# Kernel optimization log

Measured on AMD Instinct MI355X. Metric: run time of the kernel, lower is better.

The kernel has to match this reference:

```python
import jax, jax.numpy as jnp
import numpy as np
from jax import lax

N_P = 0.5      # module_cfg.n_p
CUTOFF = 0.3   # module_cfg.cutoff


def setup_inputs() -> dict:
    key = jax.random.key(0)
    k1, k2, k3, k4 = jax.random.split(key, 4)
    h = jax.random.normal(k1, (1, 8192, 256), jnp.float32)
    pos = jax.random.normal(k2, (8192, 3), jnp.float32)
    W = jax.random.normal(k3, (256, 256), jnp.float32) / 16.0  # ~ Linear init scale
    b = jax.random.normal(k4, (256,), jnp.float32) * 0.01
    return {"h": h, "pos": pos, "W": W, "b": b}


def fps_indices(pos, k, select=0):
    """Farthest point sampling; returns the k selected indices in ascending
    index order (matching torch boolean-mask indexing pos[selected])."""
    n = pos.shape[0]
    selected = jnp.zeros(n, dtype=bool).at[select].set(True)
    d = jnp.linalg.norm(pos - pos[select], axis=-1)  # (N,) euclidean, as torch.pairwise_distance
    d = jnp.where(selected, -jnp.inf, d)

    def body(i, carry):
        sel, dist = carry
        new = jnp.argmax(dist)
        sel = sel.at[new].set(True)
        dist = jnp.minimum(dist, jnp.linalg.norm(pos - pos[new], axis=-1))
        dist = jnp.where(sel, -jnp.inf, dist)
        return sel, dist

    sel, _ = lax.fori_loop(0, k - 1, body, (selected, d))
    return jnp.nonzero(sel, size=k)[0]  # exactly k True entries, sorted


def reference(h, pos, W, b):
    B, num_res, c_s = h.shape
    n_nodes = int(num_res * N_P)  # num_res * n_p // 1

    idx = fps_indices(pos, n_nodes)          # (n_nodes,)
    new_node_pos = pos[idx]                  # (n_nodes, 3)

    # torch.cdist(pos, new_node_pos, p=3): Minkowski p=3 distance
    diff = jnp.abs(pos[:, None, :] - new_node_pos[None, :, :])  # (N, n_nodes, 3)
    dist = jnp.cbrt(jnp.sum(diff ** 3, axis=-1))                 # (N, n_nodes)

    # sparse membership mask (fixed-shape equivalent of the nonzero edge list)
    mask = dist < CUTOFF                      # (N, n_nodes) bool

    # sparse gather-matmul: aggregate residue features into each sampled node
    agg = jnp.einsum('nm,bnc->bmc', mask.astype(h.dtype), h)     # (B, n_nodes, c_s)
    new_node_embed = agg @ W.T + b            # nn.Linear(c_s, c_s)
    return new_node_embed, new_node_pos, mask
```

## Files before the change

### kernel.cpp

```cpp
#include <hip/hip_runtime.h>
#include <hip/hip_bf16.h>
#include <cmath>

#define FPS_N 8192
#define FPS_K 4096
#define NTHR  1024
#define CS    256

#define NEGINF (-__builtin_inff())

__device__ __forceinline__ float p3sum(float x, float y, float z,
                                       float nx, float ny, float nz) {
  float dx = fabsf(__fsub_rn(x, nx));
  float dy = fabsf(__fsub_rn(y, ny));
  float dz = fabsf(__fsub_rn(z, nz));
  float cx = __fmul_rn(__fmul_rn(dx, dx), dx);
  float cy = __fmul_rn(__fmul_rn(dy, dy), dy);
  float cz = __fmul_rn(__fmul_rn(dz, dz), dz);
  return __fadd_rn(__fadd_rn(cx, cy), cz);
}

__device__ __forceinline__ float eucl2(float x, float y, float z,
                                       float nx, float ny, float nz) {
  float dx = __fsub_rn(x, nx);
  float dy = __fsub_rn(y, ny);
  float dz = __fsub_rn(z, nz);
  return __fadd_rn(__fadd_rn(__fmul_rn(dx, dx), __fmul_rn(dy, dy)),
                   __fmul_rn(dz, dz));
}

__global__ __launch_bounds__(NTHR) void fps_kernel(const float* __restrict__ pos,
                                                   float* __restrict__ pos_out) {
  __shared__ float rv[16];
  __shared__ int   ri[16];
  __shared__ float wposs[3];
  __shared__ int   sc[NTHR];
  const int tid  = threadIdx.x;
  const int lane = tid & 63;
  const int wave = tid >> 6;

  float x[8], y[8], z[8], d2[8], dd[8];
  {
    const float4* p4 = (const float4*)pos + tid * 6;
    float4 q0 = p4[0], q1 = p4[1], q2 = p4[2], q3 = p4[3], q4 = p4[4], q5 = p4[5];
    x[0] = q0.x; y[0] = q0.y; z[0] = q0.z;
    x[1] = q0.w; y[1] = q1.x; z[1] = q1.y;
    x[2] = q1.z; y[2] = q1.w; z[2] = q2.x;
    x[3] = q2.y; y[3] = q2.z; z[3] = q2.w;
    x[4] = q3.x; y[4] = q3.y; z[4] = q3.z;
    x[5] = q3.w; y[5] = q4.x; z[5] = q4.y;
    x[6] = q4.z; y[6] = q4.w; z[6] = q5.x;
    x[7] = q5.y; y[7] = q5.z; z[7] = q5.w;
  }
  const float p0x = pos[0], p0y = pos[1], p0z = pos[2];
#pragma unroll
  for (int j = 0; j < 8; ++j) {
    float s = eucl2(x[j], y[j], z[j], p0x, p0y, p0z);
    d2[j] = s;
    dd[j] = sqrtf(s);
  }
  if (tid == 0) { d2[0] = NEGINF; dd[0] = NEGINF; }

  float bv = 0.f; int bj = 0;
  bool chb = true;

  for (int k = 0; k < FPS_K - 1; ++k) {
    unsigned long long cb = __ballot(chb ? 1 : 0);
    if (cb != 0ULL) {
      if (chb) {
        bv = dd[0]; bj = 0;
#pragma unroll
        for (int j = 1; j < 8; ++j)
          if (dd[j] > bv) { bv = dd[j]; bj = j; }
        chb = false;
      }
      float m = bv;
#pragma unroll
      for (int off = 32; off > 0; off >>= 1)
        m = fmaxf(m, __shfl_xor(m, off));
      unsigned long long eq = __ballot((bv == m) ? 1 : 0);
      int lead = __ffsll(eq) - 1;
      int lbj  = __shfl(bj, lead);
      if (lane == 0) {
        rv[wave] = m;
        ri[wave] = ((wave << 6) + lead) * 8 + lbj;
      }
    }
    __syncthreads();

    float v  = rv[lane & 15];
    int  idx = ri[lane & 15];
#pragma unroll
    for (int off = 1; off < 16; off <<= 1) {
      float ov = __shfl_xor(v, off);
      int   oi = __shfl_xor(idx, off);
      if (ov > v || (ov == v && oi < idx)) { v = ov; idx = oi; }
    }
    const int fi = idx;

    if ((fi >> 3) == tid) {
      const int jj = fi & 7;
      float sx = x[0], sy = y[0], sz = z[0];
#pragma unroll
      for (int j = 0; j < 8; ++j)
        if (j == jj) { sx = x[j]; sy = y[j]; sz = z[j]; d2[j] = NEGINF; dd[j] = NEGINF; }
      wposs[0] = sx; wposs[1] = sy; wposs[2] = sz;
      chb = true;
    }
    __syncthreads();

    const float wx = wposs[0], wy = wposs[1], wz = wposs[2];
    unsigned cm = 0;
#pragma unroll
    for (int j = 0; j < 8; ++j) {
      float s = eucl2(x[j], y[j], z[j], wx, wy, wz);
      if (s < d2[j]) { d2[j] = s; cm |= (1u << j); }
    }
    if (cm) {
#pragma unroll
      for (int j = 0; j < 8; ++j)
        if (cm & (1u << j)) { dd[j] = sqrtf(d2[j]); if (j == bj) chb = true; }
    }
  }

  int cnt = 0;
#pragma unroll
  for (int j = 0; j < 8; ++j) cnt += (dd[j] == NEGINF) ? 1 : 0;
  sc[tid] = cnt;
  __syncthreads();
  for (int off = 1; off < NTHR; off <<= 1) {
    int vv = (tid >= off) ? sc[tid - off] : 0;
    __syncthreads();
    sc[tid] += vv;
    __syncthreads();
  }
  int base = sc[tid] - cnt;
#pragma unroll
  for (int j = 0; j < 8; ++j) {
    if (dd[j] == NEGINF) {
      pos_out[base * 3 + 0] = x[j];
      pos_out[base * 3 + 1] = y[j];
      pos_out[base * 3 + 2] = z[j];
      ++base;
    }
  }
}

__global__ __launch_bounds__(256) void wt_kernel(const float* __restrict__ W,
                                                 float* __restrict__ WT) {
  int i = blockIdx.x * 256 + threadIdx.x;
  int c = i >> 8, cp = i & 255;
  WT[i] = W[cp * 256 + c];
}

__global__ __launch_bounds__(256) void agg_linear_kernel(
    const float* __restrict__ h, const float* __restrict__ pos,
    const float* __restrict__ nodepos, const float* __restrict__ WT,
    const float* __restrict__ bias, float* __restrict__ embed, float sb) {
  const int m = blockIdx.x;
  const int tid = threadIdx.x;
  const int lane = tid & 63, wave = tid >> 6;
  const float nx = nodepos[m * 3 + 0];
  const float ny = nodepos[m * 3 + 1];
  const float nz = nodepos[m * 3 + 2];
  const float4* h4 = (const float4*)h;

  float4 acc = make_float4(0.f, 0.f, 0.f, 0.f);
  const int base0 = wave * (FPS_N / 4);
  for (int base = base0; base < base0 + (FPS_N / 4); base += 64) {
    int n = base + lane;
    float px = pos[n * 3 + 0], py = pos[n * 3 + 1], pz = pos[n * 3 + 2];
    unsigned long long mb = __ballot((p3sum(px, py, pz, nx, ny, nz) <= sb) ? 1 : 0);
    while (mb) {
      int b = __ffsll(mb) - 1;
      mb &= (mb - 1);
      float4 hv = h4[(size_t)(base + b) * 64 + lane];
      acc.x += hv.x; acc.y += hv.y; acc.z += hv.z; acc.w += hv.w;
    }
  }

  __shared__ float lacc[4][256];
  lacc[wave][lane * 4 + 0] = acc.x;
  lacc[wave][lane * 4 + 1] = acc.y;
  lacc[wave][lane * 4 + 2] = acc.z;
  lacc[wave][lane * 4 + 3] = acc.w;
  __syncthreads();
  __shared__ float aggrow[256];
  float aggv = ((lacc[0][tid] + lacc[1][tid]) + lacc[2][tid]) + lacc[3][tid];
  aggrow[tid] = aggv;
  __syncthreads();

  float o = bias[tid];
#pragma unroll 8
  for (int c = 0; c < 256; ++c)
    o = fmaf(aggrow[c], WT[c * 256 + tid], o);
  embed[(size_t)m * 256 + tid] = o;
}

__global__ __launch_bounds__(256) void mask_kernel(const float* __restrict__ pos,
                                                   const float* __restrict__ nodepos,
                                                   float* __restrict__ maskout,
                                                   float sb) {
  int n  = blockIdx.y;
  int m0 = (blockIdx.x * 256 + threadIdx.x) * 4;
  float x = pos[n * 3 + 0], y = pos[n * 3 + 1], z = pos[n * 3 + 2];
  const float4* np4 = (const float4*)(nodepos + (size_t)m0 * 3);
  float4 a = np4[0], bq = np4[1], cq = np4[2];
  float4 r;
  r.x = (p3sum(x, y, z, a.x,  a.y,  a.z)  <= sb) ? 1.0f : 0.0f;
  r.y = (p3sum(x, y, z, a.w,  bq.x, bq.y) <= sb) ? 1.0f : 0.0f;
  r.z = (p3sum(x, y, z, bq.z, bq.w, cq.x) <= sb) ? 1.0f : 0.0f;
  r.w = (p3sum(x, y, z, cq.y, cq.z, cq.w) <= sb) ? 1.0f : 0.0f;
  *(float4*)(maskout + (size_t)n * FPS_K + m0) = r;
}

extern "C" void kernel_launch(void* const* d_in, const int* in_sizes, int n_in,
                              void* d_out, int out_size, void* d_ws, size_t ws_size,
                              hipStream_t stream) {
  (void)in_sizes; (void)n_in; (void)out_size; (void)d_ws; (void)ws_size;
  const float* h   = (const float*)d_in[0];
  const float* pos = (const float*)d_in[1];
  const float* W   = (const float*)d_in[2];
  const float* b   = (const float*)d_in[3];

  float* out     = (float*)d_out;
  float* embed   = out;
  float* pos_out = out + (size_t)FPS_K * CS;
  float* mask    = pos_out + (size_t)FPS_K * 3;
  float* WT      = mask;

  const float  t    = 0.3f;
  const float  ulpv = nextafterf(t, 1.0f) - t;
  const double rmid = (double)t - (double)ulpv * 0.5;
  const double C    = rmid * rmid * rmid;
  float sb = (float)C;
  if (!((double)sb < C)) sb = nextafterf(sb, 0.0f);

  hipLaunchKernelGGL(fps_kernel, dim3(1), dim3(NTHR), 0, stream, pos, pos_out);
  hipLaunchKernelGGL(wt_kernel, dim3(256), dim3(256), 0, stream, W, WT);
  hipLaunchKernelGGL(agg_linear_kernel, dim3(FPS_K), dim3(256), 0, stream,
                     h, pos, pos_out, WT, b, embed, sb);
  hipLaunchKernelGGL(mask_kernel, dim3(4, FPS_N), dim3(256), 0, stream,
                     pos, pos_out, mask, sb);
}
```

Baseline: 7.548 ms.

## Spatially bin points for FPS and skip distance updates by bounding-box pruning

```diff
diff --git a/kernel.cpp b/kernel.cpp
--- a/kernel.cpp
+++ b/kernel.cpp
@@ -4,9 +4,9 @@
 
 #define FPS_N 8192
 #define FPS_K 4096
-#define NTHR  1024
 #define CS    256
-
+#define FT    512
+#define PPT   16
 #define NEGINF (-__builtin_inff())
 
 __device__ __forceinline__ float p3sum(float x, float y, float z,
@@ -29,119 +29,209 @@
                    __fmul_rn(dz, dz));
 }
 
-__global__ __launch_bounds__(NTHR) void fps_kernel(const float* __restrict__ pos,
-                                                   float* __restrict__ pos_out) {
-  __shared__ float rv[16];
-  __shared__ int   ri[16];
-  __shared__ float wposs[3];
-  __shared__ int   sc[NTHR];
+__global__ __launch_bounds__(FT) void bin_kernel(const float* __restrict__ pos,
+                                                 float* __restrict__ pos_s,
+                                                 int* __restrict__ ids_s) {
+  __shared__ int hist[512], cs[512], tmp[512];
+  const int tid = threadIdx.x;
+  hist[tid] = 0;
+  __syncthreads();
+
+  float qx[PPT], qy[PPT], qz[PPT];
+  int cell[PPT];
+  {
+    const float4* p4 = (const float4*)pos + tid * 12;
+#pragma unroll
+    for (int g = 0; g < 4; ++g) {
+      float4 a = p4[g * 3], b = p4[g * 3 + 1], c = p4[g * 3 + 2];
+      qx[4*g+0]=a.x; qy[4*g+0]=a.y; qz[4*g+0]=a.z;
+      qx[4*g+1]=a.w; qy[4*g+1]=b.x; qz[4*g+1]=b.y;
+      qx[4*g+2]=b.z; qy[4*g+2]=b.w; qz[4*g+2]=c.x;
+      qx[4*g+3]=c.y; qy[4*g+3]=c.z; qz[4*g+3]=c.w;
+    }
+  }
+#pragma unroll
+  for (int j = 0; j < PPT; ++j) {
+    int ix = min(max((int)floorf(qx[j] + 4.0f), 0), 7);
+    int iy = min(max((int)floorf(qy[j] + 4.0f), 0), 7);
+    int iz = min(max((int)floorf(qz[j] + 4.0f), 0), 7);
+    int m = 0;
+#pragma unroll
+    for (int b = 0; b < 3; ++b)
+      m |= (((ix >> b) & 1) << (3 * b)) | (((iy >> b) & 1) << (3 * b + 1)) |
+           (((iz >> b) & 1) << (3 * b + 2));
+    cell[j] = m;
+    atomicAdd(&hist[m], 1);
+  }
+  __syncthreads();
+  int v = hist[tid];
+  tmp[tid] = v;
+  __syncthreads();
+  for (int off = 1; off < 512; off <<= 1) {
+    int u = (tid >= off) ? tmp[tid - off] : 0;
+    __syncthreads();
+    tmp[tid] += u;
+    __syncthreads();
+  }
+  cs[tid] = tmp[tid] - v;
+  __syncthreads();
+#pragma unroll
+  for (int j = 0; j < PPT; ++j) {
+    int slot = atomicAdd(&cs[cell[j]], 1);
+    pos_s[slot * 3 + 0] = qx[j];
+    pos_s[slot * 3 + 1] = qy[j];
+    pos_s[slot * 3 + 2] = qz[j];
+    ids_s[slot] = tid * PPT + j;
+  }
+}
+
+__global__ __launch_bounds__(FT, 1) void fps_kernel(const float* __restrict__ pos,
+                                                    const float* __restrict__ pos_s,
+                                                    const int* __restrict__ ids_s,
+                                                    float* __restrict__ pos_out) {
+  __shared__ float rvv[8];
+  __shared__ int   rvk[8];
+  __shared__ float4 wposs;
+  __shared__ unsigned char flag[FPS_N];
+  __shared__ int sc[FT];
+
   const int tid  = threadIdx.x;
   const int lane = tid & 63;
   const int wave = tid >> 6;
-
-  float x[8], y[8], z[8], d2[8], dd[8];
+  const int base = tid * PPT;
+
   {
-    const float4* p4 = (const float4*)pos + tid * 6;
-    float4 q0 = p4[0], q1 = p4[1], q2 = p4[2], q3 = p4[3], q4 = p4[4], q5 = p4[5];
-    x[0] = q0.x; y[0] = q0.y; z[0] = q0.z;
-    x[1] = q0.w; y[1] = q1.x; z[1] = q1.y;
-    x[2] = q1.z; y[2] = q1.w; z[2] = q2.x;
-    x[3] = q2.y; y[3] = q2.z; z[3] = q2.w;
-    x[4] = q3.x; y[4] = q3.y; z[4] = q3.z;
-    x[5] = q3.w; y[5] = q4.x; z[5] = q4.y;
-    x[6] = q4.z; y[6] = q4.w; z[6] = q5.x;
-    x[7] = q5.y; y[7] = q5.z; z[7] = q5.w;
-  }
+    int* f4 = (int*)flag;
+#pragma unroll
+    for (int j = 0; j < 4; ++j) f4[tid * 4 + j] = 0;
+  }
+
+  float x[PPT], y[PPT], z[PPT], d2[PPT];
+  int idp[PPT / 2];
+  {
+    const float4* p4 = (const float4*)pos_s + tid * 12;
+#pragma unroll
+    for (int g = 0; g < 4; ++g) {
+      float4 a = p4[g * 3], b = p4[g * 3 + 1], c = p4[g * 3 + 2];
+      x[4*g+0]=a.x; y[4*g+0]=a.y; z[4*g+0]=a.z;
+      x[4*g+1]=a.w; y[4*g+1]=b.x; z[4*g+1]=b.y;
+      x[4*g+2]=b.z; y[4*g+2]=b.w; z[4*g+2]=c.x;
+      x[4*g+3]=c.y; y[4*g+3]=c.z; z[4*g+3]=c.w;
+    }
+    const int4* i4 = (const int4*)ids_s + tid * 4;
+#pragma unroll
+    for (int g = 0; g < 4; ++g) {
+      int4 a = i4[g];
+      idp[2 * g + 0] = (a.x & 0xffff) | (a.y << 16);
+      idp[2 * g + 1] = (a.z & 0xffff) | (a.w << 16);
+    }
+  }
+
   const float p0x = pos[0], p0y = pos[1], p0z = pos[2];
 #pragma unroll
-  for (int j = 0; j < 8; ++j) {
-    float s = eucl2(x[j], y[j], z[j], p0x, p0y, p0z);
-    d2[j] = s;
-    dd[j] = sqrtf(s);
-  }
-  if (tid == 0) { d2[0] = NEGINF; dd[0] = NEGINF; }
-
-  float bv = 0.f; int bj = 0;
-  bool chb = true;
+  for (int j = 0; j < PPT; ++j) {
+    d2[j] = eucl2(x[j], y[j], z[j], p0x, p0y, p0z);
+    int oid = (idp[j >> 1] >> ((j & 1) * 16)) & 0xffff;
+    if (oid == 0) d2[j] = NEGINF;
+  }
+  float bnx = x[0], bny = y[0], bnz = z[0], bxx = x[0], bxy = y[0], bxz = z[0];
+#pragma unroll
+  for (int j = 1; j < PPT; ++j) {
+    bnx = fminf(bnx, x[j]); bny = fminf(bny, y[j]); bnz = fminf(bnz, z[j]);
+    bxx = fmaxf(bxx, x[j]); bxy = fmaxf(bxy, y[j]); bxz = fmaxf(bxz, z[j]);
+  }
+  if (tid == 0) flag[0] = 1;
+  __syncthreads();
+
+  float bv = NEGINF;
+  int   bkey = 0x7fffffff;
+  bool  chb = true;
 
   for (int k = 0; k < FPS_K - 1; ++k) {
     unsigned long long cb = __ballot(chb ? 1 : 0);
-    if (cb != 0ULL) {
+    if (cb) {
       if (chb) {
-        bv = dd[0]; bj = 0;
-#pragma unroll
-        for (int j = 1; j < 8; ++j)
-          if (dd[j] > bv) { bv = dd[j]; bj = j; }
+        bv = NEGINF; bkey = 0x7fffffff;
+#pragma unroll
+        for (int j = 0; j < PPT; ++j) {
+          float dj = (d2[j] < 0.f) ? NEGINF : sqrtf(d2[j]);
+          int oid = (idp[j >> 1] >> ((j & 1) * 16)) & 0xffff;
+          int key = (oid << 13) | (base + j);
+          if (dj > bv || (dj == bv && key < bkey)) { bv = dj; bkey = key; }
+        }
         chb = false;
       }
-      float m = bv;
-#pragma unroll
-      for (int off = 32; off > 0; off >>= 1)
-        m = fmaxf(m, __shfl_xor(m, off));
-      unsigned long long eq = __ballot((bv == m) ? 1 : 0);
-      int lead = __ffsll(eq) - 1;
-      int lbj  = __shfl(bj, lead);
-      if (lane == 0) {
-        rv[wave] = m;
-        ri[wave] = ((wave << 6) + lead) * 8 + lbj;
+      float v = bv; int kk = bkey;
+#pragma unroll
+      for (int off = 1; off < 64; off <<= 1) {
+        float ov = __shfl_xor(v, off);
+        int   ok = __shfl_xor(kk, off);
+        if (ov > v || (ov == v && ok < kk)) { v = ov; kk = ok; }
       }
-    }
-    __syncthreads();
-
-    float v  = rv[lane & 15];
-    int  idx = ri[lane & 15];
-#pragma unroll
-    for (int off = 1; off < 16; off <<= 1) {
-      float ov = __shfl_xor(v, off);
-      int   oi = __shfl_xor(idx, off);
-      if (ov > v || (ov == v && oi < idx)) { v = ov; idx = oi; }
-    }
-    const int fi = idx;
-
-    if ((fi >> 3) == tid) {
-      const int jj = fi & 7;
+      if (lane == 0) { rvv[wave] = v; rvk[wave] = kk; }
+    }
+    __syncthreads();
+
+    float4 vv0 = *(float4*)&rvv[0]; float4 vv1 = *(float4*)&rvv[4];
+    int4   kk0 = *(int4*)&rvk[0];   int4   kk1 = *(int4*)&rvk[4];
+    float wv = vv0.x; int wk = kk0.x;
+#define CMPW(a, b) if ((a) > wv || ((a) == wv && (b) < wk)) { wv = (a); wk = (b); }
+    CMPW(vv0.y, kk0.y) CMPW(vv0.z, kk0.z) CMPW(vv0.w, kk0.w)
+    CMPW(vv1.x, kk1.x) CMPW(vv1.y, kk1.y) CMPW(vv1.z, kk1.z) CMPW(vv1.w, kk1.w)
+#undef CMPW
+    const int stor = wk & 8191;
+
+    if ((stor >> 4) == tid) {
+      const int jj = stor & 15;
       float sx = x[0], sy = y[0], sz = z[0];
 #pragma unroll
-      for (int j = 0; j < 8; ++j)
-        if (j == jj) { sx = x[j]; sy = y[j]; sz = z[j]; d2[j] = NEGINF; dd[j] = NEGINF; }
-      wposs[0] = sx; wposs[1] = sy; wposs[2] = sz;
+      for (int j = 0; j < PPT; ++j)
+        if (j == jj) { sx = x[j]; sy = y[j]; sz = z[j]; d2[j] = NEGINF; }
+      wposs = make_float4(sx, sy, sz, 0.f);
       chb = true;
     }
-    __syncthreads();
-
-    const float wx = wposs[0], wy = wposs[1], wz = wposs[2];
-    unsigned cm = 0;
-#pragma unroll
-    for (int j = 0; j < 8; ++j) {
-      float s = eucl2(x[j], y[j], z[j], wx, wy, wz);
-      if (s < d2[j]) { d2[j] = s; cm |= (1u << j); }
-    }
-    if (cm) {
-#pragma unroll
-      for (int j = 0; j < 8; ++j)
-        if (cm & (1u << j)) { dd[j] = sqrtf(d2[j]); if (j == bj) chb = true; }
-    }
-  }
-
-  int cnt = 0;
-#pragma unroll
-  for (int j = 0; j < 8; ++j) cnt += (dd[j] == NEGINF) ? 1 : 0;
+    if (tid == 0) flag[wk >> 13] = 1;
+    __syncthreads();
+
+    const float4 wp = wposs;
+    float tub = (bv < 0.f) ? NEGINF : bv * bv;
+    float cx = fminf(fmaxf(wp.x, bnx), bxx);
+    float cy = fminf(fmaxf(wp.y, bny), bxy);
+    float cz = fminf(fmaxf(wp.z, bnz), bxz);
+    float ddx = wp.x - cx, ddy = wp.y - cy, ddz = wp.z - cz;
+    float bd2 = ddx * ddx + ddy * ddy + ddz * ddz;
+    if (bd2 * 0.999f < tub) {
+#pragma unroll
+      for (int j = 0; j < PPT; ++j) {
+        float s = eucl2(x[j], y[j], z[j], wp.x, wp.y, wp.z);
+        if (s < d2[j]) { d2[j] = s; if (j == (bkey & 15)) chb = true; }
+      }
+    }
+  }
+
+  __syncthreads();
+  const int* fI = (const int*)flag;
+  int w0 = fI[tid * 4 + 0], w1 = fI[tid * 4 + 1];
+  int w2 = fI[tid * 4 + 2], w3 = fI[tid * 4 + 3];
+  int cnt = __popc(w0) + __popc(w1) + __popc(w2) + __popc(w3);
   sc[tid] = cnt;
   __syncthreads();
-  for (int off = 1; off < NTHR; off <<= 1) {
-    int vv = (tid >= off) ? sc[tid - off] : 0;
-    __syncthreads();
-    sc[tid] += vv;
-    __syncthreads();
-  }
-  int base = sc[tid] - cnt;
-#pragma unroll
-  for (int j = 0; j < 8; ++j) {
-    if (dd[j] == NEGINF) {
-      pos_out[base * 3 + 0] = x[j];
-      pos_out[base * 3 + 1] = y[j];
-      pos_out[base * 3 + 2] = z[j];
-      ++base;
+  for (int off = 1; off < FT; off <<= 1) {
+    int u = (tid >= off) ? sc[tid - off] : 0;
+    __syncthreads();
+    sc[tid] += u;
+    __syncthreads();
+  }
+  int r = sc[tid] - cnt;
+#pragma unroll
+  for (int j = 0; j < PPT; ++j) {
+    int w = (j < 4) ? w0 : (j < 8) ? w1 : (j < 12) ? w2 : w3;
+    if ((w >> ((j & 3) * 8)) & 1) {
+      int oi = tid * PPT + j;
+      pos_out[r * 3 + 0] = pos[oi * 3 + 0];
+      pos_out[r * 3 + 1] = pos[oi * 3 + 1];
+      pos_out[r * 3 + 2] = pos[oi * 3 + 2];
+      ++r;
     }
   }
 }
@@ -228,6 +318,8 @@
   float* pos_out = out + (size_t)FPS_K * CS;
   float* mask    = pos_out + (size_t)FPS_K * 3;
   float* WT      = mask;
+  float* pos_s   = mask + (1 << 21);
+  int*   ids_s   = (int*)(pos_s + 3 * FPS_N);
 
   const float  t    = 0.3f;
   const float  ulpv = nextafterf(t, 1.0f) - t;
@@ -236,7 +328,8 @@
   float sb = (float)C;
   if (!((double)sb < C)) sb = nextafterf(sb, 0.0f);
 
-  hipLaunchKernelGGL(fps_kernel, dim3(1), dim3(NTHR), 0, stream, pos, pos_out);
+  hipLaunchKernelGGL(bin_kernel, dim3(1), dim3(FT), 0, stream, pos, pos_s, ids_s);
+  hipLaunchKernelGGL(fps_kernel, dim3(1), dim3(FT), 0, stream, pos, pos_s, ids_s, pos_out);
   hipLaunchKernelGGL(wt_kernel, dim3(256), dim3(256), 0, stream, W, WT);
   hipLaunchKernelGGL(agg_linear_kernel, dim3(FPS_K), dim3(256), 0, stream,
                      h, pos, pos_out, WT, b, embed, sb);
```

Measured after the change: 13.67 ms. 81.1% more time.
